# Kernel optimization log

Measured on AMD Instinct MI355X. Metric: run time of the kernel, lower is better.

## Reference

```python
import jax, jax.numpy as jnp
import numpy as np

B, C, T = 8, 128, 8192
SIGMA_MIN = 1e-6

def setup_inputs() -> dict:
    key = jax.random.key(0)
    ks = jax.random.split(key, 9)
    x1 = jax.random.normal(ks[0], (B, C, T), dtype=jnp.float32)
    mu = jax.random.normal(ks[1], (B, C, T), dtype=jnp.float32)
    style = jax.random.normal(ks[2], (B, 192), dtype=jnp.float32)
    t_sample = jax.random.uniform(ks[3], (B, 1, 1), dtype=jnp.float32)
    z = jax.random.normal(ks[4], (B, C, T), dtype=jnp.float32)
    W = jax.random.normal(ks[5], (C, C), dtype=jnp.float32) * (1.0 / np.sqrt(C))
    b_lin = jax.random.normal(ks[6], (C,), dtype=jnp.float32) * 0.01
    prompt_lens = jax.random.randint(ks[7], (B,), 64, T // 4)
    x_lens = jax.random.randint(ks[8], (B,), T // 2, T)
    return {"x1": x1, "mu": mu, "style": style, "t_sample": t_sample, "z": z,
            "W": W, "b_lin": b_lin, "x_lens": x_lens, "prompt_lens": prompt_lens}

def reference(x1, mu, style, t_sample, z, W, b_lin, x_lens, prompt_lens):
    # x1, z: [B, C, T]; t_sample: [B, 1, 1]
    sigma = SIGMA_MIN
    Bb, Cc, Tt = x1.shape
    tpos = jnp.arange(Tt)
    pmask = tpos[None, :] < prompt_lens[:, None]            # [B, T] prompt region
    # flow-matching interpolation
    y = (1.0 - (1.0 - sigma) * t_sample) * z + t_sample * x1
    u = x1 - (1.0 - sigma) * z
    # zero out prompt region of y (prompt copy tensor is unused by the mock estimator)
    y = jnp.where(pmask[:, None, :], 0.0, y)
    # mock estimator: per-timestep Linear over channels
    out = jnp.einsum('bct,dc->bdt', y, W) + b_lin[None, :, None]
    # per-sample MSE over [prompt_lens, x_lens) across all channels, then mean over batch
    lmask = (~pmask) & (tpos[None, :] < x_lens[:, None])     # [B, T]
    diff2 = jnp.square(out - u) * lmask[:, None, :]
    counts = (Cc * jnp.sum(lmask, axis=1)).astype(x1.dtype)  # [B]
    loss = jnp.mean(jnp.sum(diff2, axis=(1, 2)) / counts)
    return loss, out + (1.0 - sigma) * z
```

## Files before the change

kernel.cpp:

```cpp
#include <hip/hip_runtime.h>
#include <hip/hip_bf16.h>

#define BB   8
#define CC   128
#define TLEN 8192
#define TBLK 32
#define NTBLK (TLEN / TBLK)
#define NBLOCKS (NTBLK * BB)
#define WS_W_OFF 8192

typedef __attribute__((ext_vector_type(8))) short short8;
typedef __attribute__((ext_vector_type(4))) float f32x4;

__device__ __forceinline__ short f2bf(float f) {
    union { float f; unsigned u; } v; v.f = f;
    return (short)((v.u + 0x7FFFu + ((v.u >> 16) & 1u)) >> 16);
}
__device__ __forceinline__ float bf2f(unsigned short h) {
    union { unsigned u; float f; } v; v.u = ((unsigned)h) << 16;
    return v.f;
}

__global__ void prep_w(const float* __restrict__ W, short* __restrict__ wsW) {
    const int gid   = blockIdx.x * 256 + threadIdx.x;
    const int lane  = gid & 63;
    const int ksdt  = gid >> 6;
    const int dtile = ksdt >> 2;
    const int ks    = ksdt & 3;
    const int row   = dtile * 16 + (lane & 15);
    const int col0  = ks * 32 + (lane >> 4) * 8;
    short8 a;
    #pragma unroll
    for (int e = 0; e < 8; ++e) a[e] = f2bf(W[row * CC + col0 + e]);
    reinterpret_cast<short8*>(wsW)[gid] = a;
}

__global__ __launch_bounds__(256, 5)
void cfm_main(const float* __restrict__ x1, const float* __restrict__ tsm,
              const float* __restrict__ z, const short* __restrict__ wsW,
              const float* __restrict__ blin, const int* __restrict__ xlens,
              const int* __restrict__ plens, float* __restrict__ out,
              float* __restrict__ wsPart)
{
    __shared__ short    ylds[TBLK][136];
    __shared__ unsigned uw[TBLK][137];
    __shared__ float    red[4];

    const int b    = blockIdx.y;
    const int t0   = blockIdx.x * TBLK;
    const int tid  = threadIdx.x;
    const int lane = tid & 63;
    const int wid  = tid >> 6;
    const int r15  = lane & 15;
    const int q4   = lane >> 4;

    const float ts  = tsm[b];
    const int   pl  = plens[b];
    const int   xl  = xlens[b];
    const float oms = 0.999999f;
    const float cz  = 1.0f - oms * ts;
    const float cx  = ts;

    short8 afrag[2][4];
    {
        const short8* wf = reinterpret_cast<const short8*>(wsW);
        #pragma unroll
        for (int dt = 0; dt < 2; ++dt)
            #pragma unroll
            for (int ks = 0; ks < 4; ++ks)
                afrag[dt][ks] = wf[((wid * 2 + dt) * 4 + ks) * 64 + lane];
    }

    {
        const int tcol = (tid & 7) * 4;
        const int crow = tid >> 3;
        #pragma unroll
        for (int p = 0; p < 4; ++p) {
            const int c = p * 32 + crow;
            const size_t g = (size_t)(b * CC + c) * TLEN + t0 + tcol;
            const float4 xv = *reinterpret_cast<const float4*>(x1 + g);
            const float4 zv = *reinterpret_cast<const float4*>(z + g);
            const float xa[4] = {xv.x, xv.y, xv.z, xv.w};
            const float za[4] = {zv.x, zv.y, zv.z, zv.w};
            #pragma unroll
            for (int j = 0; j < 4; ++j) {
                const int t = t0 + tcol + j;
                float y = cz * za[j] + cx * xa[j];
                if (t < pl) y = 0.0f;
                ylds[tcol + j][c] = f2bf(y);
                const float w = oms * za[j];
                const float u = xa[j] - w;
                uw[tcol + j][c] = (unsigned)(unsigned short)f2bf(u)
                                | ((unsigned)(unsigned short)f2bf(w) << 16);
            }
        }
    }
    __syncthreads();

    f32x4 acc[2][2];
    #pragma unroll
    for (int dt = 0; dt < 2; ++dt)
        #pragma unroll
        for (int tt = 0; tt < 2; ++tt)
            acc[dt][tt] = (f32x4){0.f, 0.f, 0.f, 0.f};

    #pragma unroll
    for (int ks = 0; ks < 4; ++ks) {
        #pragma unroll
        for (int tt = 0; tt < 2; ++tt) {
            const short8 bfrag =
                *reinterpret_cast<const short8*>(&ylds[tt * 16 + r15][ks * 32 + q4 * 8]);
            acc[0][tt] = __builtin_amdgcn_mfma_f32_16x16x32_bf16(afrag[0][ks], bfrag, acc[0][tt], 0, 0, 0);
            acc[1][tt] = __builtin_amdgcn_mfma_f32_16x16x32_bf16(afrag[1][ks], bfrag, acc[1][tt], 0, 0, 0);
        }
    }

    float bl[2][4];
    #pragma unroll
    for (int dt = 0; dt < 2; ++dt)
        #pragma unroll
        for (int rr = 0; rr < 4; ++rr)
            bl[dt][rr] = blin[wid * 32 + dt * 16 + q4 * 4 + rr];

    float lsum = 0.0f;
    #pragma unroll
    for (int dt = 0; dt < 2; ++dt) {
        #pragma unroll
        for (int tt = 0; tt < 2; ++tt) {
            const int tl = tt * 16 + r15;
            const int t  = t0 + tl;
            const bool lm = (t >= pl) & (t < xl);
            #pragma unroll
            for (int rr = 0; rr < 4; ++rr) {
                const int d = wid * 32 + dt * 16 + q4 * 4 + rr;
                const unsigned uwv = uw[tl][d];
                const float u = bf2f((unsigned short)(uwv & 0xFFFFu));
                const float w = bf2f((unsigned short)(uwv >> 16));
                const float ov = acc[dt][tt][rr] + bl[dt][rr];
                out[1 + (size_t)(b * CC + d) * TLEN + t] = ov + w;
                if (lm) { const float df = ov - u; lsum += df * df; }
            }
        }
    }

    #pragma unroll
    for (int off = 32; off >= 1; off >>= 1) lsum += __shfl_down(lsum, off);
    if (lane == 0) red[wid] = lsum;
    __syncthreads();
    if (tid == 0) {
        const float scale = 1.0f / (1024.0f * (float)(xl - pl));
        wsPart[blockIdx.y * gridDim.x + blockIdx.x] =
            (red[0] + red[1] + red[2] + red[3]) * scale;
    }
}

__global__ void final_red(const float* __restrict__ wsPart, float* __restrict__ out) {
    __shared__ float red[4];
    const int tid = threadIdx.x;
    float s = 0.0f;
    #pragma unroll
    for (int i = 0; i < NBLOCKS / 256; ++i) s += wsPart[tid + i * 256];
    #pragma unroll
    for (int off = 32; off >= 1; off >>= 1) s += __shfl_down(s, off);
    if ((tid & 63) == 0) red[tid >> 6] = s;
    __syncthreads();
    if (tid == 0) out[0] = red[0] + red[1] + red[2] + red[3];
}

extern "C" void kernel_launch(void* const* d_in, const int* in_sizes, int n_in,
                              void* d_out, int out_size, void* d_ws, size_t ws_size,
                              hipStream_t stream) {
    const float* x1    = (const float*)d_in[0];
    const float* tsm   = (const float*)d_in[3];
    const float* z     = (const float*)d_in[4];
    const float* W     = (const float*)d_in[5];
    const float* blin  = (const float*)d_in[6];
    const int*   xlens = (const int*)d_in[7];
    const int*   plens = (const int*)d_in[8];
    float* out = (float*)d_out;

    float* wsPart = (float*)d_ws;
    short* wsW    = (short*)((char*)d_ws + WS_W_OFF);

    prep_w<<<8, 256, 0, stream>>>(W, wsW);
    dim3 grid(NTBLK, BB);
    cfm_main<<<grid, 256, 0, stream>>>(x1, tsm, z, wsW, blin, xlens, plens, out, wsPart);
    final_red<<<1, 256, 0, stream>>>(wsPart, out);
}
```

Baseline: 31.59 us.

## Stage raw x1/z tiles in LDS and split GEMM into two MFMA passes

Instead of building the interpolated y tile and packed u/w in shared memory, the kernel stores bf16 copies of x1 and z. It runs separate MFMAs on each and combines them afterwards as cx*Wx + cz*Wz, applying the prompt mask after the GEMM. All global loads are issued before the LDS writes, and the two output-row tiles are computed and stored one after the other to lower register pressure. Launch bounds rise to 8 waves per SIMD for higher occupancy, at the cost of doubling the MFMA count.

```diff
diff --git a/kernel.cpp b/kernel.cpp
--- a/kernel.cpp
+++ b/kernel.cpp
@@ -35,16 +35,16 @@
     reinterpret_cast<short8*>(wsW)[gid] = a;
 }
 
-__global__ __launch_bounds__(256, 5)
+__global__ __launch_bounds__(256, 8)
 void cfm_main(const float* __restrict__ x1, const float* __restrict__ tsm,
               const float* __restrict__ z, const short* __restrict__ wsW,
               const float* __restrict__ blin, const int* __restrict__ xlens,
               const int* __restrict__ plens, float* __restrict__ out,
               float* __restrict__ wsPart)
 {
-    __shared__ short    ylds[TBLK][136];
-    __shared__ unsigned uw[TBLK][137];
-    __shared__ float    red[4];
+    __shared__ short xt[TBLK][136];
+    __shared__ short zt[TBLK][136];
+    __shared__ float red[4];
 
     const int b    = blockIdx.y;
     const int t0   = blockIdx.x * TBLK;
@@ -61,84 +61,113 @@
     const float cz  = 1.0f - oms * ts;
     const float cx  = ts;
 
-    short8 afrag[2][4];
-    {
-        const short8* wf = reinterpret_cast<const short8*>(wsW);
-        #pragma unroll
-        for (int dt = 0; dt < 2; ++dt)
-            #pragma unroll
-            for (int ks = 0; ks < 4; ++ks)
-                afrag[dt][ks] = wf[((wid * 2 + dt) * 4 + ks) * 64 + lane];
-    }
-
-    {
-        const int tcol = (tid & 7) * 4;
-        const int crow = tid >> 3;
-        #pragma unroll
-        for (int p = 0; p < 4; ++p) {
-            const int c = p * 32 + crow;
-            const size_t g = (size_t)(b * CC + c) * TLEN + t0 + tcol;
-            const float4 xv = *reinterpret_cast<const float4*>(x1 + g);
-            const float4 zv = *reinterpret_cast<const float4*>(z + g);
-            const float xa[4] = {xv.x, xv.y, xv.z, xv.w};
-            const float za[4] = {zv.x, zv.y, zv.z, zv.w};
-            #pragma unroll
-            for (int j = 0; j < 4; ++j) {
-                const int t = t0 + tcol + j;
-                float y = cz * za[j] + cx * xa[j];
-                if (t < pl) y = 0.0f;
-                ylds[tcol + j][c] = f2bf(y);
-                const float w = oms * za[j];
-                const float u = xa[j] - w;
-                uw[tcol + j][c] = (unsigned)(unsigned short)f2bf(u)
-                                | ((unsigned)(unsigned short)f2bf(w) << 16);
-            }
+    const short8* wf = reinterpret_cast<const short8*>(wsW);
+
+    const int tcol = (tid & 7) * 4;
+    const int crow = tid >> 3;
+    const size_t gbase = (size_t)b * CC * TLEN + (size_t)t0 + tcol;
+
+    float4 xv[4], zv[4];
+    #pragma unroll
+    for (int p = 0; p < 4; ++p)
+        xv[p] = *reinterpret_cast<const float4*>(x1 + gbase + (size_t)(p * 32 + crow) * TLEN);
+    #pragma unroll
+    for (int p = 0; p < 4; ++p)
+        zv[p] = *reinterpret_cast<const float4*>(z + gbase + (size_t)(p * 32 + crow) * TLEN);
+
+    short8 af0[4];
+    #pragma unroll
+    for (int ks = 0; ks < 4; ++ks)
+        af0[ks] = wf[((wid * 2 + 0) * 4 + ks) * 64 + lane];
+
+    #pragma unroll
+    for (int p = 0; p < 4; ++p) {
+        const int c = p * 32 + crow;
+        const float* xs = reinterpret_cast<const float*>(&xv[p]);
+        const float* zs = reinterpret_cast<const float*>(&zv[p]);
+        #pragma unroll
+        for (int j = 0; j < 4; ++j) {
+            xt[tcol + j][c] = f2bf(xs[j]);
+            zt[tcol + j][c] = f2bf(zs[j]);
         }
     }
     __syncthreads();
 
-    f32x4 acc[2][2];
-    #pragma unroll
-    for (int dt = 0; dt < 2; ++dt)
-        #pragma unroll
-        for (int tt = 0; tt < 2; ++tt)
-            acc[dt][tt] = (f32x4){0.f, 0.f, 0.f, 0.f};
-
-    #pragma unroll
-    for (int ks = 0; ks < 4; ++ks) {
-        #pragma unroll
-        for (int tt = 0; tt < 2; ++tt) {
-            const short8 bfrag =
-                *reinterpret_cast<const short8*>(&ylds[tt * 16 + r15][ks * 32 + q4 * 8]);
-            acc[0][tt] = __builtin_amdgcn_mfma_f32_16x16x32_bf16(afrag[0][ks], bfrag, acc[0][tt], 0, 0, 0);
-            acc[1][tt] = __builtin_amdgcn_mfma_f32_16x16x32_bf16(afrag[1][ks], bfrag, acc[1][tt], 0, 0, 0);
-        }
-    }
-
-    float bl[2][4];
-    #pragma unroll
-    for (int dt = 0; dt < 2; ++dt)
-        #pragma unroll
-        for (int rr = 0; rr < 4; ++rr)
-            bl[dt][rr] = blin[wid * 32 + dt * 16 + q4 * 4 + rr];
-
     float lsum = 0.0f;
-    #pragma unroll
-    for (int dt = 0; dt < 2; ++dt) {
+
+    {
+        short8 af1[4];
+        #pragma unroll
+        for (int ks = 0; ks < 4; ++ks)
+            af1[ks] = wf[((wid * 2 + 1) * 4 + ks) * 64 + lane];
+
+        f32x4 ax[2], az[2];
+        #pragma unroll
+        for (int tt = 0; tt < 2; ++tt) { ax[tt] = (f32x4){0,0,0,0}; az[tt] = (f32x4){0,0,0,0}; }
+
+        #pragma unroll
+        for (int ks = 0; ks < 4; ++ks) {
+            #pragma unroll
+            for (int tt = 0; tt < 2; ++tt) {
+                const short8 xf = *reinterpret_cast<const short8*>(&xt[tt * 16 + r15][ks * 32 + q4 * 8]);
+                const short8 zf = *reinterpret_cast<const short8*>(&zt[tt * 16 + r15][ks * 32 + q4 * 8]);
+                ax[tt] = __builtin_amdgcn_mfma_f32_16x16x32_bf16(af0[ks], xf, ax[tt], 0, 0, 0);
+                az[tt] = __builtin_amdgcn_mfma_f32_16x16x32_bf16(af0[ks], zf, az[tt], 0, 0, 0);
+            }
+        }
+
         #pragma unroll
         for (int tt = 0; tt < 2; ++tt) {
             const int tl = tt * 16 + r15;
             const int t  = t0 + tl;
-            const bool lm = (t >= pl) & (t < xl);
+            const bool pm = (t >= pl);
+            const bool lm = pm & (t < xl);
             #pragma unroll
             for (int rr = 0; rr < 4; ++rr) {
-                const int d = wid * 32 + dt * 16 + q4 * 4 + rr;
-                const unsigned uwv = uw[tl][d];
-                const float u = bf2f((unsigned short)(uwv & 0xFFFFu));
-                const float w = bf2f((unsigned short)(uwv >> 16));
-                const float ov = acc[dt][tt][rr] + bl[dt][rr];
+                const int d = wid * 32 + q4 * 4 + rr;
+                const float bl = blin[d];
+                const float zf = bf2f((unsigned short)zt[tl][d]);
+                const float xf = bf2f((unsigned short)xt[tl][d]);
+                const float w  = oms * zf;
+                const float s  = cx * ax[tt][rr] + cz * az[tt][rr];
+                const float ov = (pm ? s : 0.0f) + bl;
                 out[1 + (size_t)(b * CC + d) * TLEN + t] = ov + w;
-                if (lm) { const float df = ov - u; lsum += df * df; }
+                if (lm) { const float df = ov - (xf - w); lsum += df * df; }
+            }
+        }
+
+        f32x4 bx[2], bz[2];
+        #pragma unroll
+        for (int tt = 0; tt < 2; ++tt) { bx[tt] = (f32x4){0,0,0,0}; bz[tt] = (f32x4){0,0,0,0}; }
+
+        #pragma unroll
+        for (int ks = 0; ks < 4; ++ks) {
+            #pragma unroll
+            for (int tt = 0; tt < 2; ++tt) {
+                const short8 xf = *reinterpret_cast<const short8*>(&xt[tt * 16 + r15][ks * 32 + q4 * 8]);
+                const short8 zf = *reinterpret_cast<const short8*>(&zt[tt * 16 + r15][ks * 32 + q4 * 8]);
+                bx[tt] = __builtin_amdgcn_mfma_f32_16x16x32_bf16(af1[ks], xf, bx[tt], 0, 0, 0);
+                bz[tt] = __builtin_amdgcn_mfma_f32_16x16x32_bf16(af1[ks], zf, bz[tt], 0, 0, 0);
+            }
+        }
+
+        #pragma unroll
+        for (int tt = 0; tt < 2; ++tt) {
+            const int tl = tt * 16 + r15;
+            const int t  = t0 + tl;
+            const bool pm = (t >= pl);
+            const bool lm = pm & (t < xl);
+            #pragma unroll
+            for (int rr = 0; rr < 4; ++rr) {
+                const int d = wid * 32 + 16 + q4 * 4 + rr;
+                const float bl = blin[d];
+                const float zf = bf2f((unsigned short)zt[tl][d]);
+                const float xf = bf2f((unsigned short)xt[tl][d]);
+                const float w  = oms * zf;
+                const float s  = cx * bx[tt][rr] + cz * bz[tt][rr];
+                const float ov = (pm ? s : 0.0f) + bl;
+                out[1 + (size_t)(b * CC + d) * TLEN + t] = ov + w;
+                if (lm) { const float df = ov - (xf - w); lsum += df * df; }
             }
         }
     }
```

Result: slower. 32.77 us (+3.7%).

## Process two time tiles per block with prefetch, swizzled LDS, separate x/z GEMMs

Applied to the files above, without the earlier changes.

Each block now handles 64 timesteps as two 32-step tiles, issuing the global loads for the second tile before computing the first, so memory latency overlaps with MFMA work. x1 and z are stored raw as bf16 in XOR-swizzled LDS and multiplied by W separately, with the interpolation coefficients and prompt mask applied after the GEMM. The epilogue now maps timesteps so each lane writes along t, and u and w are rebuilt from the stored bf16 inputs. This doubles the MFMA count, halves the grid, and lowers the occupancy hint. It also changes where rounding happens, since the loss now uses bf16-rounded x and z.

```diff
diff --git a/kernel.cpp b/kernel.cpp
--- a/kernel.cpp
+++ b/kernel.cpp
@@ -5,8 +5,7 @@
 #define CC   128
 #define TLEN 8192
 #define TBLK 32
-#define NTBLK (TLEN / TBLK)
-#define NBLOCKS (NTBLK * BB)
+#define NB   1024
 #define WS_W_OFF 8192
 
 typedef __attribute__((ext_vector_type(8))) short short8;
@@ -19,6 +18,9 @@
 __device__ __forceinline__ float bf2f(unsigned short h) {
     union { unsigned u; float f; } v; v.u = ((unsigned)h) << 16;
     return v.f;
+}
+__device__ __forceinline__ int swz(int t, int c) {
+    return c ^ (((t ^ (t >> 2)) & 7) << 3);
 }
 
 __global__ void prep_w(const float* __restrict__ W, short* __restrict__ wsW) {
@@ -35,19 +37,80 @@
     reinterpret_cast<short8*>(wsW)[gid] = a;
 }
 
-__global__ __launch_bounds__(256, 5)
+__device__ __forceinline__ void compute_tile(
+    const short (*xb)[CC], const short (*zb)[CC], const short8 (&af)[2][4],
+    int wid, int r15, int q4, int tcur, int b, int pl, int xl,
+    float cx, float cz, float oms, const float* __restrict__ blin,
+    float* __restrict__ out, float& lsum)
+{
+    f32x4 aX[2][2], aZ[2][2];
+    #pragma unroll
+    for (int dt = 0; dt < 2; ++dt)
+        #pragma unroll
+        for (int tt = 0; tt < 2; ++tt) {
+            aX[dt][tt] = (f32x4){0.f, 0.f, 0.f, 0.f};
+            aZ[dt][tt] = (f32x4){0.f, 0.f, 0.f, 0.f};
+        }
+
+    #pragma unroll
+    for (int ks = 0; ks < 4; ++ks) {
+        #pragma unroll
+        for (int tt = 0; tt < 2; ++tt) {
+            const int tr = tt * 16 + r15;
+            const int cs = swz(tr, ks * 32 + q4 * 8);
+            const short8 xa = *reinterpret_cast<const short8*>(&xb[tr][cs]);
+            const short8 za = *reinterpret_cast<const short8*>(&zb[tr][cs]);
+            #pragma unroll
+            for (int dt = 0; dt < 2; ++dt) {
+                aX[dt][tt] = __builtin_amdgcn_mfma_f32_16x16x32_bf16(xa, af[dt][ks], aX[dt][tt], 0, 0, 0);
+                aZ[dt][tt] = __builtin_amdgcn_mfma_f32_16x16x32_bf16(za, af[dt][ks], aZ[dt][tt], 0, 0, 0);
+            }
+        }
+    }
+
+    #pragma unroll
+    for (int dt = 0; dt < 2; ++dt) {
+        const int d  = wid * 32 + dt * 16 + r15;
+        const float bl = blin[d];
+        float* orow = out + 1 + (size_t)(b * CC + d) * TLEN;
+        #pragma unroll
+        for (int tt = 0; tt < 2; ++tt) {
+            const int tb = tt * 16 + q4 * 4;
+            #pragma unroll
+            for (int j = 0; j < 4; ++j) {
+                const int tl = tb + j;
+                const int tg = tcur + tl;
+                const float s  = cx * aX[dt][tt][j] + cz * aZ[dt][tt][j];
+                const bool pm  = tg >= pl;
+                const float ov = (pm ? s : 0.0f) + bl;
+                const float zf = bf2f((unsigned short)zb[tl][swz(tl, d)]);
+                const float w  = oms * zf;
+                orow[tg] = ov + w;
+                if (pm & (tg < xl)) {
+                    const float xf = bf2f((unsigned short)xb[tl][swz(tl, d)]);
+                    const float df = ov - (xf - w);
+                    lsum += df * df;
+                }
+            }
+        }
+    }
+}
+
+__global__ __launch_bounds__(256, 4)
 void cfm_main(const float* __restrict__ x1, const float* __restrict__ tsm,
               const float* __restrict__ z, const short* __restrict__ wsW,
               const float* __restrict__ blin, const int* __restrict__ xlens,
               const int* __restrict__ plens, float* __restrict__ out,
               float* __restrict__ wsPart)
 {
-    __shared__ short    ylds[TBLK][136];
-    __shared__ unsigned uw[TBLK][137];
-    __shared__ float    red[4];
-
-    const int b    = blockIdx.y;
-    const int t0   = blockIdx.x * TBLK;
+    __shared__ short xt[2][TBLK][CC];
+    __shared__ short zt[2][TBLK][CC];
+    __shared__ float red[4];
+
+    const int bi = blockIdx.x;
+    const int b  = bi & 7;
+    const int t0 = (bi >> 3) * 64;
+
     const int tid  = threadIdx.x;
     const int lane = tid & 63;
     const int wid  = tid >> 6;
@@ -61,87 +124,68 @@
     const float cz  = 1.0f - oms * ts;
     const float cx  = ts;
 
-    short8 afrag[2][4];
+    short8 af[2][4];
     {
         const short8* wf = reinterpret_cast<const short8*>(wsW);
         #pragma unroll
         for (int dt = 0; dt < 2; ++dt)
             #pragma unroll
             for (int ks = 0; ks < 4; ++ks)
-                afrag[dt][ks] = wf[((wid * 2 + dt) * 4 + ks) * 64 + lane];
-    }
-
-    {
-        const int tcol = (tid & 7) * 4;
-        const int crow = tid >> 3;
-        #pragma unroll
-        for (int p = 0; p < 4; ++p) {
-            const int c = p * 32 + crow;
-            const size_t g = (size_t)(b * CC + c) * TLEN + t0 + tcol;
-            const float4 xv = *reinterpret_cast<const float4*>(x1 + g);
-            const float4 zv = *reinterpret_cast<const float4*>(z + g);
-            const float xa[4] = {xv.x, xv.y, xv.z, xv.w};
-            const float za[4] = {zv.x, zv.y, zv.z, zv.w};
-            #pragma unroll
-            for (int j = 0; j < 4; ++j) {
-                const int t = t0 + tcol + j;
-                float y = cz * za[j] + cx * xa[j];
-                if (t < pl) y = 0.0f;
-                ylds[tcol + j][c] = f2bf(y);
-                const float w = oms * za[j];
-                const float u = xa[j] - w;
-                uw[tcol + j][c] = (unsigned)(unsigned short)f2bf(u)
-                                | ((unsigned)(unsigned short)f2bf(w) << 16);
-            }
-        }
-    }
-    __syncthreads();
-
-    f32x4 acc[2][2];
-    #pragma unroll
-    for (int dt = 0; dt < 2; ++dt)
-        #pragma unroll
-        for (int tt = 0; tt < 2; ++tt)
-            acc[dt][tt] = (f32x4){0.f, 0.f, 0.f, 0.f};
-
-    #pragma unroll
-    for (int ks = 0; ks < 4; ++ks) {
-        #pragma unroll
-        for (int tt = 0; tt < 2; ++tt) {
-            const short8 bfrag =
-                *reinterpret_cast<const short8*>(&ylds[tt * 16 + r15][ks * 32 + q4 * 8]);
-            acc[0][tt] = __builtin_amdgcn_mfma_f32_16x16x32_bf16(afrag[0][ks], bfrag, acc[0][tt], 0, 0, 0);
-            acc[1][tt] = __builtin_amdgcn_mfma_f32_16x16x32_bf16(afrag[1][ks], bfrag, acc[1][tt], 0, 0, 0);
-        }
-    }
-
-    float bl[2][4];
-    #pragma unroll
-    for (int dt = 0; dt < 2; ++dt)
-        #pragma unroll
-        for (int rr = 0; rr < 4; ++rr)
-            bl[dt][rr] = blin[wid * 32 + dt * 16 + q4 * 4 + rr];
-
+                af[dt][ks] = wf[((wid * 2 + dt) * 4 + ks) * 64 + lane];
+    }
+
+    const int tj = (tid & 7) * 4;
+    const int cr = tid >> 3;
+    const size_t rowb = (size_t)b * CC * TLEN;
+
+    float4 xv[4], zv[4];
     float lsum = 0.0f;
-    #pragma unroll
-    for (int dt = 0; dt < 2; ++dt) {
-        #pragma unroll
-        for (int tt = 0; tt < 2; ++tt) {
-            const int tl = tt * 16 + r15;
-            const int t  = t0 + tl;
-            const bool lm = (t >= pl) & (t < xl);
-            #pragma unroll
-            for (int rr = 0; rr < 4; ++rr) {
-                const int d = wid * 32 + dt * 16 + q4 * 4 + rr;
-                const unsigned uwv = uw[tl][d];
-                const float u = bf2f((unsigned short)(uwv & 0xFFFFu));
-                const float w = bf2f((unsigned short)(uwv >> 16));
-                const float ov = acc[dt][tt][rr] + bl[dt][rr];
-                out[1 + (size_t)(b * CC + d) * TLEN + t] = ov + w;
-                if (lm) { const float df = ov - u; lsum += df * df; }
-            }
-        }
-    }
+
+    #pragma unroll
+    for (int p = 0; p < 4; ++p) {
+        const size_t g = rowb + (size_t)(p * 32 + cr) * TLEN + t0 + tj;
+        xv[p] = *reinterpret_cast<const float4*>(x1 + g);
+        zv[p] = *reinterpret_cast<const float4*>(z + g);
+    }
+    #pragma unroll
+    for (int p = 0; p < 4; ++p) {
+        const int c = p * 32 + cr;
+        const float* xs = reinterpret_cast<const float*>(&xv[p]);
+        const float* zs = reinterpret_cast<const float*>(&zv[p]);
+        #pragma unroll
+        for (int j = 0; j < 4; ++j) {
+            const int t = tj + j;
+            const int cs = swz(t, c);
+            xt[0][t][cs] = f2bf(xs[j]);
+            zt[0][t][cs] = f2bf(zs[j]);
+        }
+    }
+    #pragma unroll
+    for (int p = 0; p < 4; ++p) {
+        const size_t g = rowb + (size_t)(p * 32 + cr) * TLEN + t0 + 32 + tj;
+        xv[p] = *reinterpret_cast<const float4*>(x1 + g);
+        zv[p] = *reinterpret_cast<const float4*>(z + g);
+    }
+    __syncthreads();
+
+    compute_tile(xt[0], zt[0], af, wid, r15, q4, t0, b, pl, xl, cx, cz, oms, blin, out, lsum);
+
+    #pragma unroll
+    for (int p = 0; p < 4; ++p) {
+        const int c = p * 32 + cr;
+        const float* xs = reinterpret_cast<const float*>(&xv[p]);
+        const float* zs = reinterpret_cast<const float*>(&zv[p]);
+        #pragma unroll
+        for (int j = 0; j < 4; ++j) {
+            const int t = tj + j;
+            const int cs = swz(t, c);
+            xt[1][t][cs] = f2bf(xs[j]);
+            zt[1][t][cs] = f2bf(zs[j]);
+        }
+    }
+    __syncthreads();
+
+    compute_tile(xt[1], zt[1], af, wid, r15, q4, t0 + 32, b, pl, xl, cx, cz, oms, blin, out, lsum);
 
     #pragma unroll
     for (int off = 32; off >= 1; off >>= 1) lsum += __shfl_down(lsum, off);
@@ -149,8 +193,7 @@
     __syncthreads();
     if (tid == 0) {
         const float scale = 1.0f / (1024.0f * (float)(xl - pl));
-        wsPart[blockIdx.y * gridDim.x + blockIdx.x] =
-            (red[0] + red[1] + red[2] + red[3]) * scale;
+        wsPart[bi] = (red[0] + red[1] + red[2] + red[3]) * scale;
     }
 }
 
@@ -159,7 +202,7 @@
     const int tid = threadIdx.x;
     float s = 0.0f;
     #pragma unroll
-    for (int i = 0; i < NBLOCKS / 256; ++i) s += wsPart[tid + i * 256];
+    for (int i = 0; i < NB / 256; ++i) s += wsPart[tid + i * 256];
     #pragma unroll
     for (int off = 32; off >= 1; off >>= 1) s += __shfl_down(s, off);
     if ((tid & 63) == 0) red[tid >> 6] = s;
@@ -183,7 +226,6 @@
     short* wsW    = (short*)((char*)d_ws + WS_W_OFF);
 
     prep_w<<<8, 256, 0, stream>>>(W, wsW);
-    dim3 grid(NTBLK, BB);
-    cfm_main<<<grid, 256, 0, stream>>>(x1, tsm, z, wsW, blin, xlens, plens, out, wsPart);
+    cfm_main<<<NB, 256, 0, stream>>>(x1, tsm, z, wsW, blin, xlens, plens, out, wsPart);
     final_red<<<1, 256, 0, stream>>>(wsPart, out);
 }
```

Result: slower. 57.11 us (+80.8%).

## Run separate GEMMs on x1 and z, combine with scalars, larger swizzled tiles

Applied to the files above, without the earlier changes.

The kernel stops building y in registers before the matmul. It stores bf16 copies of x1 and z in XOR-swizzled shared memory, runs two MFMA GEMMs (W·x1 and W·z) and combines them with cx and cz afterwards. The time tile grows from 32 to 128 with 512 threads, each wave owns 16 output channels, all global loads are issued up front, and the grid becomes 1D with batch interleaved. This doubles the MFMA work but lowers LDS bank conflicts and per-block overhead and exposes more memory-level parallelism. The final output no longer needs the separate u/w buffer.

```diff
diff --git a/kernel.cpp b/kernel.cpp
--- a/kernel.cpp
+++ b/kernel.cpp
@@ -4,9 +4,8 @@
 #define BB   8
 #define CC   128
 #define TLEN 8192
-#define TBLK 32
-#define NTBLK (TLEN / TBLK)
-#define NBLOCKS (NTBLK * BB)
+#define TBLK 128
+#define NB   (BB * (TLEN / TBLK))
 #define WS_W_OFF 8192
 
 typedef __attribute__((ext_vector_type(8))) short short8;
@@ -19,6 +18,9 @@
 __device__ __forceinline__ float bf2f(unsigned short h) {
     union { unsigned u; float f; } v; v.u = ((unsigned)h) << 16;
     return v.f;
+}
+__device__ __forceinline__ int swz(int t, int c) {
+    return c ^ (((t ^ (t >> 3)) & 15) << 3);
 }
 
 __global__ void prep_w(const float* __restrict__ W, short* __restrict__ wsW) {
@@ -35,19 +37,21 @@
     reinterpret_cast<short8*>(wsW)[gid] = a;
 }
 
-__global__ __launch_bounds__(256, 5)
+__global__ __launch_bounds__(512, 4)
 void cfm_main(const float* __restrict__ x1, const float* __restrict__ tsm,
               const float* __restrict__ z, const short* __restrict__ wsW,
               const float* __restrict__ blin, const int* __restrict__ xlens,
               const int* __restrict__ plens, float* __restrict__ out,
               float* __restrict__ wsPart)
 {
-    __shared__ short    ylds[TBLK][136];
-    __shared__ unsigned uw[TBLK][137];
-    __shared__ float    red[4];
+    __shared__ short xt[TBLK][CC];
+    __shared__ short zt[TBLK][CC];
+    __shared__ float red[8];
 
-    const int b    = blockIdx.y;
-    const int t0   = blockIdx.x * TBLK;
+    const int bi = blockIdx.x;
+    const int b  = bi & 7;
+    const int t0 = (bi >> 3) * TBLK;
+
     const int tid  = threadIdx.x;
     const int lane = tid & 63;
     const int wid  = tid >> 6;
@@ -61,84 +65,78 @@
     const float cz  = 1.0f - oms * ts;
     const float cx  = ts;
 
-    short8 afrag[2][4];
+    const int tpart = (tid & 31) * 4;
+    const int c0    = tid >> 5;
+    const size_t rowb = (size_t)b * CC * TLEN + (size_t)t0 + tpart;
+
+    float4 xv[8], zv[8];
+    #pragma unroll
+    for (int p = 0; p < 8; ++p)
+        xv[p] = *reinterpret_cast<const float4*>(x1 + rowb + (size_t)(c0 + p * 16) * TLEN);
+    #pragma unroll
+    for (int p = 0; p < 8; ++p)
+        zv[p] = *reinterpret_cast<const float4*>(z + rowb + (size_t)(c0 + p * 16) * TLEN);
+
+    short8 af[4];
     {
         const short8* wf = reinterpret_cast<const short8*>(wsW);
         #pragma unroll
-        for (int dt = 0; dt < 2; ++dt)
-            #pragma unroll
-            for (int ks = 0; ks < 4; ++ks)
-                afrag[dt][ks] = wf[((wid * 2 + dt) * 4 + ks) * 64 + lane];
+        for (int ks = 0; ks < 4; ++ks)
+            af[ks] = wf[(wid * 4 + ks) * 64 + lane];
     }
 
-    {
-        const int tcol = (tid & 7) * 4;
-        const int crow = tid >> 3;
+    #pragma unroll
+    for (int p = 0; p < 8; ++p) {
+        const int c = c0 + p * 16;
+        const float* xs = reinterpret_cast<const float*>(&xv[p]);
+        const float* zs = reinterpret_cast<const float*>(&zv[p]);
         #pragma unroll
-        for (int p = 0; p < 4; ++p) {
-            const int c = p * 32 + crow;
-            const size_t g = (size_t)(b * CC + c) * TLEN + t0 + tcol;
-            const float4 xv = *reinterpret_cast<const float4*>(x1 + g);
-            const float4 zv = *reinterpret_cast<const float4*>(z + g);
-            const float xa[4] = {xv.x, xv.y, xv.z, xv.w};
-            const float za[4] = {zv.x, zv.y, zv.z, zv.w};
-            #pragma unroll
-            for (int j = 0; j < 4; ++j) {
-                const int t = t0 + tcol + j;
-                float y = cz * za[j] + cx * xa[j];
-                if (t < pl) y = 0.0f;
-                ylds[tcol + j][c] = f2bf(y);
-                const float w = oms * za[j];
-                const float u = xa[j] - w;
-                uw[tcol + j][c] = (unsigned)(unsigned short)f2bf(u)
-                                | ((unsigned)(unsigned short)f2bf(w) << 16);
-            }
+        for (int j = 0; j < 4; ++j) {
+            const int t  = tpart + j;
+            const int cs = swz(t, c);
+            xt[t][cs] = f2bf(xs[j]);
+            zt[t][cs] = f2bf(zs[j]);
         }
     }
     __syncthreads();
 
-    f32x4 acc[2][2];
+    f32x4 aX[8], aZ[8];
     #pragma unroll
-    for (int dt = 0; dt < 2; ++dt)
-        #pragma unroll
-        for (int tt = 0; tt < 2; ++tt)
-            acc[dt][tt] = (f32x4){0.f, 0.f, 0.f, 0.f};
+    for (int tt = 0; tt < 8; ++tt) { aX[tt] = (f32x4){0,0,0,0}; aZ[tt] = (f32x4){0,0,0,0}; }
 
     #pragma unroll
     for (int ks = 0; ks < 4; ++ks) {
         #pragma unroll
-        for (int tt = 0; tt < 2; ++tt) {
-            const short8 bfrag =
-                *reinterpret_cast<const short8*>(&ylds[tt * 16 + r15][ks * 32 + q4 * 8]);
-            acc[0][tt] = __builtin_amdgcn_mfma_f32_16x16x32_bf16(afrag[0][ks], bfrag, acc[0][tt], 0, 0, 0);
-            acc[1][tt] = __builtin_amdgcn_mfma_f32_16x16x32_bf16(afrag[1][ks], bfrag, acc[1][tt], 0, 0, 0);
+        for (int tt = 0; tt < 8; ++tt) {
+            const int tr = tt * 16 + r15;
+            const int cs = swz(tr, ks * 32 + q4 * 8);
+            const short8 xa = *reinterpret_cast<const short8*>(&xt[tr][cs]);
+            const short8 za = *reinterpret_cast<const short8*>(&zt[tr][cs]);
+            aX[tt] = __builtin_amdgcn_mfma_f32_16x16x32_bf16(af[ks], xa, aX[tt], 0, 0, 0);
+            aZ[tt] = __builtin_amdgcn_mfma_f32_16x16x32_bf16(af[ks], za, aZ[tt], 0, 0, 0);
         }
     }
 
-    float bl[2][4];
-    #pragma unroll
-    for (int dt = 0; dt < 2; ++dt)
-        #pragma unroll
-        for (int rr = 0; rr < 4; ++rr)
-            bl[dt][rr] = blin[wid * 32 + dt * 16 + q4 * 4 + rr];
-
     float lsum = 0.0f;
     #pragma unroll
-    for (int dt = 0; dt < 2; ++dt) {
+    for (int rr = 0; rr < 4; ++rr) {
+        const int d  = wid * 16 + q4 * 4 + rr;
+        const float bl = blin[d];
+        float* orow = out + 1 + (size_t)(b * CC + d) * TLEN + t0;
         #pragma unroll
-        for (int tt = 0; tt < 2; ++tt) {
+        for (int tt = 0; tt < 8; ++tt) {
             const int tl = tt * 16 + r15;
-            const int t  = t0 + tl;
-            const bool lm = (t >= pl) & (t < xl);
-            #pragma unroll
-            for (int rr = 0; rr < 4; ++rr) {
-                const int d = wid * 32 + dt * 16 + q4 * 4 + rr;
-                const unsigned uwv = uw[tl][d];
-                const float u = bf2f((unsigned short)(uwv & 0xFFFFu));
-                const float w = bf2f((unsigned short)(uwv >> 16));
-                const float ov = acc[dt][tt][rr] + bl[dt][rr];
-                out[1 + (size_t)(b * CC + d) * TLEN + t] = ov + w;
-                if (lm) { const float df = ov - u; lsum += df * df; }
+            const int tg = t0 + tl;
+            const float s  = cx * aX[tt][rr] + cz * aZ[tt][rr];
+            const bool pm  = tg >= pl;
+            const float ov = (pm ? s : 0.0f) + bl;
+            const int cs   = swz(tl, d);
+            const float w  = oms * bf2f((unsigned short)zt[tl][cs]);
+            orow[tl] = ov + w;
+            if (pm & (tg < xl)) {
+                const float xf = bf2f((unsigned short)xt[tl][cs]);
+                const float df = ov - (xf - w);
+                lsum += df * df;
             }
         }
     }
@@ -149,8 +147,10 @@
     __syncthreads();
     if (tid == 0) {
         const float scale = 1.0f / (1024.0f * (float)(xl - pl));
-        wsPart[blockIdx.y * gridDim.x + blockIdx.x] =
-            (red[0] + red[1] + red[2] + red[3]) * scale;
+        float s = 0.0f;
+        #pragma unroll
+        for (int w = 0; w < 8; ++w) s += red[w];
+        wsPart[bi] = s * scale;
     }
 }
 
@@ -159,7 +159,7 @@
     const int tid = threadIdx.x;
     float s = 0.0f;
     #pragma unroll
-    for (int i = 0; i < NBLOCKS / 256; ++i) s += wsPart[tid + i * 256];
+    for (int i = 0; i < NB / 256; ++i) s += wsPart[tid + i * 256];
     #pragma unroll
     for (int off = 32; off >= 1; off >>= 1) s += __shfl_down(s, off);
     if ((tid & 63) == 0) red[tid >> 6] = s;
@@ -183,7 +183,6 @@
     short* wsW    = (short*)((char*)d_ws + WS_W_OFF);
 
     prep_w<<<8, 256, 0, stream>>>(W, wsW);
-    dim3 grid(NTBLK, BB);
-    cfm_main<<<grid, 256, 0, stream>>>(x1, tsm, z, wsW, blin, xlens, plens, out, wsPart);
+    cfm_main<<<NB, 512, 0, stream>>>(x1, tsm, z, wsW, blin, xlens, plens, out, wsPart);
     final_red<<<1, 256, 0, stream>>>(wsPart, out);
 }
```

After: 31.09 us. No clear change (-1.6%).
